# Kernel optimization log

Measured on AMD Instinct MI355X. Metric: run time of the kernel, lower is better.

## Reference

```python
import jax, jax.numpy as jnp
import numpy as np

K = 7            # neighbor volumes (NNN heads)
PS = 10          # patch size
ADJ = PS // 2    # patch anchor offset (use_adj)
WOFF = 29 // 2   # search window half-size (ws=29)
KSEARCH = 224    # hardcoded in forward
T, C, E, HH, WW = 1, 8, 8, 64, 64


def _box1(a, axis):
    # sliding-window sum of length PS anchored at i-ADJ, zero outside
    pw = [(0, 0)] * a.ndim
    pw[axis] = (ADJ, PS - 1 - ADJ)
    ap = jnp.pad(a, pw)
    c = jnp.cumsum(ap, axis=axis)
    zp = [(0, 0)] * a.ndim
    zp[axis] = (1, 0)
    c = jnp.pad(c, zp)
    n = a.shape[axis]
    return jax.lax.slice_in_dim(c, PS, PS + n, axis=axis) - jax.lax.slice_in_dim(c, 0, n, axis=axis)


def box_sum(a):
    return _box1(_box1(a, -2), -1)


def setup_inputs():
    key = jax.random.key(0)
    ks = jax.random.split(key, 5)
    x = jax.random.normal(ks[0], (T, C, HH, WW), jnp.float32)
    xe = jax.random.normal(ks[1], (T, E, HH, WW), jnp.float32)
    ye = jax.random.normal(ks[2], (T, E, HH, WW), jnp.float32)
    y = jax.random.normal(ks[3], (T, C, HH, WW), jnp.float32)
    log_temp = 0.1 * jax.random.normal(ks[4], (T, 1, HH, WW), jnp.float32)
    return {"x": x, "xe": xe, "ye": ye, "y": y, "log_temp": log_temp}


def reference(x, xe, ye, y, log_temp):
    pad = lambda a: jnp.pad(a, ((0, 0), (0, 0), (1, 1), (1, 1)))
    x, xe, ye, y, log_temp = pad(x), pad(xe), pad(ye), pad(y), pad(log_temp)
    H, W = x.shape[-2:]
    Q = H * W
    xe0, ye0 = xe[0], ye[0]
    # search window offsets (ws x ws)
    dy, dx = np.meshgrid(np.arange(-WOFF, WOFF + 1), np.arange(-WOFF, WOFF + 1), indexing='ij')
    dy = jnp.asarray(dy.ravel()); dx = jnp.asarray(dx.ravel())
    nW = dy.shape[0]  # 841
    # patch squared norms (zero padded patches)
    n2_q = box_sum((ye0 ** 2).sum(0))   # (H,W)
    n2_db = box_sum((xe0 ** 2).sum(0))  # (H,W)
    xep = jnp.pad(xe0, ((0, 0), (WOFF, WOFF), (WOFF, WOFF)))
    n2p = jnp.pad(n2_db, WOFF)
    def shifted(d):
        s = jax.lax.dynamic_slice(xep, (0, WOFF + d[0], WOFF + d[1]), (E, H, W))
        n = jax.lax.dynamic_slice(n2p, (WOFF + d[0], WOFF + d[1]), (H, W))
        return s, n
    xe_s, n2_s = jax.vmap(shifted)(jnp.stack([dy, dx], -1))  # (nW,E,H,W),(nW,H,W)
    cross = box_sum((ye0[None] * xe_s).sum(1))               # (nW,H,W)
    dist = n2_q[None] + n2_s - 2.0 * cross                   # L2^2, (nW,H,W)
    qy = jnp.arange(H)[:, None]; qx = jnp.arange(W)[None, :]
    valid = ((qy[None] + dy[:, None, None] >= 0) & (qy[None] + dy[:, None, None] < H)
             & (qx[None] + dx[:, None, None] >= 0) & (qx[None] + dx[:, None, None] < W))
    self_m = (dy == 0) & (dx == 0)  # remove_self
    dist = jnp.where(valid & ~self_m[:, None, None], dist, 1e10)
    dist = dist.transpose(1, 2, 0).reshape(Q, nW)
    negd, idx = jax.lax.top_k(-dist, KSEARCH)  # closest KSEARCH, negd = -L2
    # avg-pooled log temperature per query patch
    lt = (box_sum(log_temp[0, 0]) / (PS * PS)).reshape(Q)
    # NeuralNearestNeighbors: iterative continuous top-k relaxation
    logits = negd / jnp.exp(lt)[:, None]
    Ws = []
    for _ in range(K):
        w = jax.nn.softmax(logits, axis=-1)
        logits = logits + jnp.log(jnp.clip(1.0 - w, 1e-6, None))
        Ws.append(w)
    Wk = jnp.stack(Ws)  # (K,Q,KSEARCH)
    # absolute candidate coords
    qyf = jnp.repeat(jnp.arange(H), W); qxf = jnp.tile(jnp.arange(W), H)
    ny = qyf[:, None] + dy[idx]; nx = qxf[:, None] + dx[idx]  # (Q,KSEARCH)
    # weighted patch sum (gather per patch offset)
    xpad = jnp.pad(x[0], ((0, 0), (ADJ, PS - 1 - ADJ), (ADJ, PS - 1 - ADJ)))
    z = jnp.zeros((K, Q, C, PS, PS), x.dtype)
    for oy in range(PS):
        for ox in range(PS):
            vals = xpad[:, ny + oy, nx + ox]  # (C,Q,KSEARCH)
            z = z.at[:, :, :, oy, ox].set(jnp.einsum('kqj,cqj->kqc', Wk, vals))
    # fold with counting (iFoldz): overlap-add of patches + coverage counts
    zp = z.transpose(1, 0, 2, 3, 4).reshape(H, W, K * C, PS, PS)
    buf = jnp.zeros((K * C, H + PS - 1, W + PS - 1), x.dtype)
    cnt = jnp.zeros((H + PS - 1, W + PS - 1), x.dtype)
    for oy in range(PS):
        for ox in range(PS):
            buf = buf.at[:, oy:oy + H, ox:ox + W].add(zp[:, :, :, oy, ox].transpose(2, 0, 1))
            cnt = cnt.at[oy:oy + H, ox:ox + W].add(1.0)
    vid = buf[:, ADJ:ADJ + H, ADJ:ADJ + W]
    zvid = cnt[ADJ:ADJ + H, ADJ:ADJ + W]
    zagg = vid / zvid[None]
    zagg = zagg.reshape(T, K, C, H, W) - y.reshape(T, 1, C, H, W)
    zagg = zagg.reshape(T, K * C, H, W)
    out = jnp.concatenate([y, zagg], axis=1)[..., 1:-1, 1:-1]
    return out
```

## Files before the change

kernel.cpp:

```cpp
#include <hip/hip_runtime.h>
#include <hip/hip_bf16.h>

#define HP    66
#define QTOT  (HP*HP)
#define LSTR  67
#define NWIN  29
#define NW    (NWIN*NWIN)
#define KK    7
#define WOFF2 14
#define NZ    15
#define QB    8
#define QBN   545
#define NIT   27
#define NSEG3 198


__global__ __launch_bounds__(256) void k_prep1(const float* __restrict__ x,
    const float* __restrict__ xe, const float* __restrict__ ye,
    const float* __restrict__ lt, float* __restrict__ ws) {
  int p = blockIdx.x * 256 + threadIdx.x;
  if (p >= QTOT) return;
  int i = p / HP, j = p % HP;
  bool in = (i >= 1 && i < HP-1 && j >= 1 && j < HP-1);
  int src = (i-1)*64 + (j-1);
  float vy[8], vx[8], vv[8];
  float sy = 0.f, sx = 0.f;
#pragma unroll
  for (int e = 0; e < 8; ++e) {
    vy[e] = in ? ye[e*4096 + src] : 0.f;
    vx[e] = in ? xe[e*4096 + src] : 0.f;
    vv[e] = in ? x [e*4096 + src] : 0.f;
    sy += vy[e]*vy[e]; sx += vx[e]*vx[e];
  }
  float4* yp = (float4*)(ws + (size_t)p*8);
  float4* xp = (float4*)(ws + 8*QTOT + (size_t)p*8);
  float4* vp = (float4*)(ws + 16*QTOT + (size_t)p*8);
  yp[0] = make_float4(vy[0], vy[1], vy[2], vy[3]);
  yp[1] = make_float4(vy[4], vy[5], vy[6], vy[7]);
  xp[0] = make_float4(vx[0], vx[1], vx[2], vx[3]);
  xp[1] = make_float4(vx[4], vx[5], vx[6], vx[7]);
  vp[0] = make_float4(vv[0], vv[1], vv[2], vv[3]);
  vp[1] = make_float4(vv[4], vv[5], vv[6], vv[7]);
  ws[24*QTOT + p] = sy;
  ws[25*QTOT + p] = sx;
  ws[26*QTOT + p] = in ? lt[src] : 0.f;
}

__global__ __launch_bounds__(256) void k_prep2(float* __restrict__ ws) {
  int p = blockIdx.x * 256 + threadIdx.x;
  if (p >= QTOT) return;
  int i = p / HP, j = p % HP;
  const float* sqye = ws + 24*QTOT;
  const float* sqxe = ws + 25*QTOT;
  const float* lt66 = ws + 26*QTOT;
  float a = 0.f, b = 0.f, c = 0.f;
  for (int u = -5; u <= 4; ++u) {
    int ii = i + u; if (ii < 0 || ii >= HP) continue;
    for (int v = -5; v <= 4; ++v) {
      int jj = j + v; if (jj < 0 || jj >= HP) continue;
      int o = ii*HP + jj;
      a += sqye[o]; b += sqxe[o]; c += lt66[o];
    }
  }
  ws[27*QTOT + p] = a;
  ws[28*QTOT + p] = b;
  ws[29*QTOT + p] = c * 0.01f;
}

__global__ __launch_bounds__(256) void k_dist(const float* __restrict__ ws,
                                              float* __restrict__ dist) {
  __shared__ float s[HP*LSTR];
  __shared__ float h[HP*LSTR];
  int w = blockIdx.x, tid = threadIdx.x;
  int dy = w / NWIN - WOFF2, dx = w % NWIN - WOFF2;
  const float* yex = ws;
  const float* xex = ws + 8*QTOT;
  const float* n2q  = ws + 27*QTOT;
  const float* n2db = ws + 28*QTOT;
  for (int p = tid; p < QTOT; p += 256) {
    int i = p / HP, j = p % HP;
    int ii = i + dy, jj = j + dx;
    float sv = 0.f;
    if (ii >= 0 && ii < HP && jj >= 0 && jj < HP) {
      int p2 = ii*HP + jj;
      const float4* yp = (const float4*)(yex + (size_t)p*8);
      const float4* xp = (const float4*)(xex + (size_t)p2*8);
      float4 a0 = yp[0], a1 = yp[1], b0 = xp[0], b1 = xp[1];
      sv += a0.x*b0.x; sv += a0.y*b0.y; sv += a0.z*b0.z; sv += a0.w*b0.w;
      sv += a1.x*b1.x; sv += a1.y*b1.y; sv += a1.z*b1.z; sv += a1.w*b1.w;
    }
    s[i*LSTR + j] = sv;
  }
  __syncthreads();
  if (tid < NSEG3) {
    int row = tid % HP, seg = tid / HP, c0 = seg*22;
    const float* ar = s + row*LSTR;
    float* hr = h + row*LSTR;
    float w9[9]; float sum = 0.f;
#pragma unroll
    for (int t = 0; t < 9; ++t) {
      int jj = c0 - 5 + t;
      float v = (jj >= 0) ? ar[jj] : 0.f;
      w9[t] = v; sum += v;
    }
#pragma unroll
    for (int t = 0; t < 22; ++t) {
      int j = c0 + t, jn = j + 4;
      float nv = (jn < HP) ? ar[jn] : 0.f;
      sum += nv;
      hr[j] = sum;
      sum -= w9[t % 9];
      w9[t % 9] = nv;
    }
  }
  __syncthreads();
  if (tid < NSEG3) {
    int col = tid % HP, seg = tid / HP, r0 = seg*22;
    float w9[9]; float sum = 0.f;
#pragma unroll
    for (int t = 0; t < 9; ++t) {
      int ii = r0 - 5 + t;
      float v = (ii >= 0) ? h[ii*LSTR + col] : 0.f;
      w9[t] = v; sum += v;
    }
#pragma unroll
    for (int t = 0; t < 22; ++t) {
      int i = r0 + t, in2 = i + 4;
      float nv = (in2 < HP) ? h[in2*LSTR + col] : 0.f;
      sum += nv;
      float cr = sum;
      int p = i*HP + col;
      int ii = i + dy, jj = col + dx;
      bool valid = (ii >= 0 && ii < HP && jj >= 0 && jj < HP);
      float dv = 1e10f;
      if (valid && !(dy == 0 && dx == 0))
        dv = n2q[p] + n2db[ii*HP + jj] - 2.f * cr;
      dist[w*QTOT + p] = dv;
      sum -= w9[t % 9];
      w9[t % 9] = nv;
    }
  }
}

__global__ __launch_bounds__(256) void k_weights(const float* __restrict__ ws,
    const float* __restrict__ dist, __hip_bfloat16* __restrict__ wf) {
  __shared__ float mh[32], sh[32];
  int tid = threadIdx.x;
  int qq = tid & (QB-1);
  int qb = blockIdx.x;
  int q = qb * QB + qq;
  bool qok = q < QTOT;
  int qs = qok ? q : (QTOT - 1);
  int wg = tid >> 3;
  int wave = tid >> 6;
  float invT = __expf(-ws[29*QTOT + qs]);
  float lv[NIT];
#pragma unroll
  for (int it = 0; it < NIT; ++it) {
    int w = wg + it*32;
    lv[it] = (qok && w < NW) ? (-dist[w*QTOT + qs] * invT) : -3.0e38f;
  }
  for (int k = 0; k < KK; ++k) {
    float pm = -3.0e38f;
#pragma unroll
    for (int it = 0; it < NIT; ++it) pm = fmaxf(pm, lv[it]);
    pm = fmaxf(pm, __shfl_xor(pm, 8, 64));
    pm = fmaxf(pm, __shfl_xor(pm, 16, 64));
    pm = fmaxf(pm, __shfl_xor(pm, 32, 64));
    if ((tid & 63) < QB) mh[wave*QB + qq] = pm;
    __syncthreads();
    float m = fmaxf(fmaxf(mh[qq], mh[QB+qq]), fmaxf(mh[2*QB+qq], mh[3*QB+qq]));
    float psum = 0.f;
#pragma unroll
    for (int it = 0; it < NIT; ++it) psum += __expf(lv[it] - m);
    psum += __shfl_xor(psum, 8, 64);
    psum += __shfl_xor(psum, 16, 64);
    psum += __shfl_xor(psum, 32, 64);
    if ((tid & 63) < QB) sh[wave*QB + qq] = psum;
    __syncthreads();
    float invden = 1.0f / (sh[qq] + sh[QB+qq] + sh[2*QB+qq] + sh[3*QB+qq]);
    size_t bkq = ((size_t)k*QBN + qb)*NW;
#pragma unroll
    for (int it = 0; it < NIT; ++it) {
      int w = wg + it*32;
      if (qok && w < NW) {
        float wgt = __expf(lv[it] - m) * invden;
        wf[(bkq + w)*8 + qq] = __float2bfloat16(wgt);
        if (k < KK-1 && wgt > 1e-9f)
          lv[it] += __logf(fmaxf(1.f - wgt, 1e-6f));
      }
    }
    __syncthreads();
  }
}

__global__ __launch_bounds__(256) void k_boxw(__hip_bfloat16* __restrict__ wfp) {
  __shared__ uint4 au4[546];
  __shared__ float h[QTOT];
  int bid = blockIdx.x;
  int l = (bid & 7)*736 + (bid >> 3);
  if (l >= KK*NW) return;
  int k = l / NW, w = l % NW;
  uint4* u4 = (uint4*)wfp;
  size_t pb = ((size_t)k*QBN)*NW + w;
  int tid = threadIdx.x;
  for (int qb = tid; qb < QBN; qb += 256)
    au4[qb] = u4[pb + (size_t)qb*NW];
  if (tid < 8) ((unsigned short*)au4)[4356 + tid] = 0;
  __syncthreads();
  const unsigned short* a16 = (const unsigned short*)au4;
  if (tid < NSEG3) {
    int row = tid % HP, seg = tid / HP, c0 = seg*22;
    const unsigned short* ar = a16 + row*HP;
    float* hr = h + row*HP;
    float w9[9]; float sum = 0.f;
#pragma unroll
    for (int t = 0; t < 9; ++t) {
      int jj = c0 - 4 + t;
      float v = (jj >= 0) ? __uint_as_float((unsigned)ar[jj] << 16) : 0.f;
      w9[t] = v; sum += v;
    }
#pragma unroll
    for (int t = 0; t < 22; ++t) {
      int j = c0 + t, jn = j + 5;
      float nv = (jn < HP) ? __uint_as_float((unsigned)ar[jn] << 16) : 0.f;
      sum += nv;
      hr[j] = sum;
      sum -= w9[t % 9];
      w9[t % 9] = nv;
    }
  }
  __syncthreads();
  unsigned short* a16w = (unsigned short*)au4;
  if (tid < NSEG3) {
    int col = tid % HP, seg = tid / HP, r0 = seg*22;
    float w9[9]; float sum = 0.f;
#pragma unroll
    for (int t = 0; t < 9; ++t) {
      int ii = r0 - 4 + t;
      float v = (ii >= 0) ? h[ii*HP + col] : 0.f;
      w9[t] = v; sum += v;
    }
#pragma unroll
    for (int t = 0; t < 22; ++t) {
      int i = r0 + t, in2 = i + 5;
      float nv = (in2 < HP) ? h[in2*HP + col] : 0.f;
      sum += nv;
      a16w[i*HP + col] = __bfloat16_as_ushort(__float2bfloat16(sum));
      sum -= w9[t % 9];
      w9[t % 9] = nv;
    }
  }
  __syncthreads();
  for (int qb = tid; qb < QBN; qb += 256)
    u4[pb + (size_t)qb*NW] = au4[qb];
}

__global__ __launch_bounds__(256) void k_contract(const float* __restrict__ ws,
    const unsigned short* __restrict__ wfu, float* __restrict__ accb2) {
  __shared__ float xt[17][44][8];
  int t = blockIdx.x, z = blockIdx.y, k = blockIdx.z, tid = threadIdx.x;
  int I0 = (t >> 2) * 16, J0 = (t & 3) * 16;
  int dylo = -WOFF2 + 2*z;
  int gy0 = I0 + 1 + dylo, gx0 = J0 - 13;
  const float* x66i = ws + 16*QTOT;
  for (int idx = tid; idx < 17*44; idx += 256) {
    int r = idx / 44, cc = idx % 44;
    int gy = gy0 + r, gx = gx0 + cc;
    float4 v0 = make_float4(0.f,0.f,0.f,0.f), v1 = v0;
    if (gy >= 0 && gy < HP && gx >= 0 && gx < HP) {
      const float4* xp = (const float4*)(x66i + (size_t)(gy*HP + gx)*8);
      v0 = xp[0]; v1 = xp[1];
    }
    float4* d = (float4*)&xt[r][cc][0];
    d[0] = v0; d[1] = v1;
  }
  __syncthreads();
  int il = tid >> 4, jl = tid & 15;
  int I = I0 + 1 + il, J = J0 + 1 + jl;
  int pix = I*HP + J;
  int qb = pix >> 3, q7 = pix & 7;
  size_t cb = (((size_t)k*QBN + qb)*NW)*8 + q7;
  float acc[8];
#pragma unroll
  for (int c = 0; c < 8; ++c) acc[c] = 0.f;
  int ndd = (z == NZ-1) ? 1 : 2;
  for (int dd = 0; dd < ndd; ++dd) {
    int wrow = (dylo + dd + WOFF2) * NWIN;
    const unsigned short* wp = wfu + cb + (size_t)wrow*8;
    unsigned short wv[NWIN];
#pragma unroll
    for (int dxw = 0; dxw < NWIN; ++dxw) wv[dxw] = wp[dxw*8];
    int r = il + dd;
#pragma unroll
    for (int dxw = 0; dxw < NWIN; ++dxw) {
      float wgt = __uint_as_float((unsigned)wv[dxw] << 16);
      const float4* xr = (const float4*)&xt[r][jl + dxw][0];
      float4 x0 = xr[0], x1 = xr[1];
      acc[0] += wgt * x0.x; acc[1] += wgt * x0.y;
      acc[2] += wgt * x0.z; acc[3] += wgt * x0.w;
      acc[4] += wgt * x1.x; acc[5] += wgt * x1.y;
      acc[6] += wgt * x1.z; acc[7] += wgt * x1.w;
    }
  }
  int px64 = (I-1)*64 + (J-1);
#pragma unroll
  for (int c = 0; c < 8; ++c)
    accb2[((z*56 + k*8 + c)*4096) + px64] = acc[c];
}

__global__ __launch_bounds__(256) void k_final(const float* __restrict__ y,
    const float* __restrict__ accb2, float* __restrict__ out) {
  int idx = blockIdx.x * 256 + threadIdx.x;
  int ch = idx >> 12, px = idx & 4095;
  if (ch < 8) { out[idx] = y[ch*4096 + px]; return; }
  int kc = ch - 8, c = kc & 7;
  int i = px >> 6, j = px & 63;
  int I = i + 1, J = j + 1;
  int cy = min(I+5, HP-1) - max(I-4, 0) + 1;
  int cx = min(J+5, HP-1) - max(J-4, 0) + 1;
  float s = 0.f;
  for (int z = 0; z < NZ; ++z) s += accb2[(z*56 + kc)*4096 + px];
  out[idx] = s / (float)(cy*cx) - y[c*4096 + px];
}

extern "C" void kernel_launch(void* const* d_in, const int* in_sizes, int n_in,
                              void* d_out, int out_size, void* d_ws, size_t ws_size,
                              hipStream_t stream) {
  const float* x  = (const float*)d_in[0];
  const float* xe = (const float*)d_in[1];
  const float* ye = (const float*)d_in[2];
  const float* y  = (const float*)d_in[3];
  const float* lt = (const float*)d_in[4];
  float* ws   = (float*)d_ws;
  float* dist = ws + 30*QTOT;
  __hip_bfloat16* wf = (__hip_bfloat16*)(dist + (size_t)NW*QTOT);
  float* accb2 = dist;
  float* out = (float*)d_out;

  k_prep1<<<(QTOT + 255)/256, 256, 0, stream>>>(x, xe, ye, lt, ws);
  k_prep2<<<(QTOT + 255)/256, 256, 0, stream>>>(ws);
  k_dist<<<NW, 256, 0, stream>>>(ws, dist);
  k_weights<<<QBN, 256, 0, stream>>>(ws, dist, wf);
  k_boxw<<<KK*NW, 256, 0, stream>>>(wf);
  k_contract<<<dim3(16, NZ, KK), 256, 0, stream>>>(ws, (const unsigned short*)wf, accb2);
  k_final<<<out_size/256, 256, 0, stream>>>(y, accb2, out);
}
```

Measured before the change: 145.9 us.

## Batch four window offsets per k_boxw block with padded weight layout

The weight buffer's per-query-block stride is padded from 841 to 844 window offsets, with the padding zeroed in k_weights. Each k_boxw block now processes four adjacent offsets, so its global loads and stores cover 64 contiguous bytes instead of scattered 16-byte chunks, and the launch shrinks to about a quarter of the blocks. In exchange each block holds four planes in LDS (about 35 KB plus the float plane), which lowers occupancy, and it runs the four box filters one after another with extra barriers.

```diff
diff --git a/kernel.cpp b/kernel.cpp
--- a/kernel.cpp
+++ b/kernel.cpp
@@ -6,6 +6,8 @@
 #define LSTR  67
 #define NWIN  29
 #define NW    (NWIN*NWIN)
+#define NWP   844
+#define NG    211
 #define KK    7
 #define WOFF2 14
 #define NZ    15
@@ -153,6 +155,12 @@
   int qs = qok ? q : (QTOT - 1);
   int wg = tid >> 3;
   int wave = tid >> 6;
+  if (tid < 24) {
+    int wp2 = NW + (tid >> 3), q2 = tid & 7;
+#pragma unroll
+    for (int k = 0; k < KK; ++k)
+      wf[(((size_t)k*QBN + qb)*NWP + wp2)*8 + q2] = __float2bfloat16(0.f);
+  }
   float invT = __expf(-ws[29*QTOT + qs]);
   float lv[NIT];
 #pragma unroll
@@ -179,7 +187,7 @@
     if ((tid & 63) < QB) sh[wave*QB + qq] = psum;
     __syncthreads();
     float invden = 1.0f / (sh[qq] + sh[QB+qq] + sh[2*QB+qq] + sh[3*QB+qq]);
-    size_t bkq = ((size_t)k*QBN + qb)*NW;
+    size_t bkq = ((size_t)k*QBN + qb)*NWP;
 #pragma unroll
     for (int it = 0; it < NIT; ++it) {
       int w = wg + it*32;
@@ -195,65 +203,74 @@
 }
 
 __global__ __launch_bounds__(256) void k_boxw(__hip_bfloat16* __restrict__ wfp) {
-  __shared__ uint4 au4[546];
+  __shared__ uint4 au4[4][546];
   __shared__ float h[QTOT];
   int bid = blockIdx.x;
-  int l = (bid & 7)*736 + (bid >> 3);
-  if (l >= KK*NW) return;
-  int k = l / NW, w = l % NW;
+  int k = bid / NG, g = bid % NG;
+  int w0 = g * 4;
   uint4* u4 = (uint4*)wfp;
-  size_t pb = ((size_t)k*QBN)*NW + w;
+  size_t pb = ((size_t)k*QBN)*NWP + w0;
   int tid = threadIdx.x;
-  for (int qb = tid; qb < QBN; qb += 256)
-    au4[qb] = u4[pb + (size_t)qb*NW];
-  if (tid < 8) ((unsigned short*)au4)[4356 + tid] = 0;
+  for (int idx = tid; idx < QBN*4; idx += 256) {
+    int qb = idx >> 2, wl = idx & 3;
+    au4[wl][qb] = u4[pb + (size_t)qb*NWP + wl];
+  }
+  if (tid < 48) {
+    int pl = tid / 12, e = tid % 12;
+    ((unsigned short*)au4[pl])[4356 + e] = 0;
+  }
   __syncthreads();
-  const unsigned short* a16 = (const unsigned short*)au4;
-  if (tid < NSEG3) {
-    int row = tid % HP, seg = tid / HP, c0 = seg*22;
-    const unsigned short* ar = a16 + row*HP;
-    float* hr = h + row*HP;
-    float w9[9]; float sum = 0.f;
-#pragma unroll
-    for (int t = 0; t < 9; ++t) {
-      int jj = c0 - 4 + t;
-      float v = (jj >= 0) ? __uint_as_float((unsigned)ar[jj] << 16) : 0.f;
-      w9[t] = v; sum += v;
-    }
-#pragma unroll
-    for (int t = 0; t < 22; ++t) {
-      int j = c0 + t, jn = j + 5;
-      float nv = (jn < HP) ? __uint_as_float((unsigned)ar[jn] << 16) : 0.f;
-      sum += nv;
-      hr[j] = sum;
-      sum -= w9[t % 9];
-      w9[t % 9] = nv;
-    }
-  }
-  __syncthreads();
-  unsigned short* a16w = (unsigned short*)au4;
-  if (tid < NSEG3) {
-    int col = tid % HP, seg = tid / HP, r0 = seg*22;
-    float w9[9]; float sum = 0.f;
-#pragma unroll
-    for (int t = 0; t < 9; ++t) {
-      int ii = r0 - 4 + t;
-      float v = (ii >= 0) ? h[ii*HP + col] : 0.f;
-      w9[t] = v; sum += v;
-    }
-#pragma unroll
-    for (int t = 0; t < 22; ++t) {
-      int i = r0 + t, in2 = i + 5;
-      float nv = (in2 < HP) ? h[in2*HP + col] : 0.f;
-      sum += nv;
-      a16w[i*HP + col] = __bfloat16_as_ushort(__float2bfloat16(sum));
-      sum -= w9[t % 9];
-      w9[t % 9] = nv;
-    }
-  }
-  __syncthreads();
-  for (int qb = tid; qb < QBN; qb += 256)
-    u4[pb + (size_t)qb*NW] = au4[qb];
+#pragma unroll
+  for (int pl = 0; pl < 4; ++pl) {
+    const unsigned short* a16 = (const unsigned short*)au4[pl];
+    if (tid < NSEG3) {
+      int row = tid % HP, seg = tid / HP, c0 = seg*22;
+      const unsigned short* ar = a16 + row*HP;
+      float* hr = h + row*HP;
+      float w9[9]; float sum = 0.f;
+#pragma unroll
+      for (int t = 0; t < 9; ++t) {
+        int jj = c0 - 4 + t;
+        float v = (jj >= 0) ? __uint_as_float((unsigned)ar[jj] << 16) : 0.f;
+        w9[t] = v; sum += v;
+      }
+#pragma unroll
+      for (int t = 0; t < 22; ++t) {
+        int j = c0 + t, jn = j + 5;
+        float nv = (jn < HP) ? __uint_as_float((unsigned)ar[jn] << 16) : 0.f;
+        sum += nv;
+        hr[j] = sum;
+        sum -= w9[t % 9];
+        w9[t % 9] = nv;
+      }
+    }
+    __syncthreads();
+    unsigned short* a16w = (unsigned short*)au4[pl];
+    if (tid < NSEG3) {
+      int col = tid % HP, seg = tid / HP, r0 = seg*22;
+      float w9[9]; float sum = 0.f;
+#pragma unroll
+      for (int t = 0; t < 9; ++t) {
+        int ii = r0 - 4 + t;
+        float v = (ii >= 0) ? h[ii*HP + col] : 0.f;
+        w9[t] = v; sum += v;
+      }
+#pragma unroll
+      for (int t = 0; t < 22; ++t) {
+        int i = r0 + t, in2 = i + 5;
+        float nv = (in2 < HP) ? h[in2*HP + col] : 0.f;
+        sum += nv;
+        a16w[i*HP + col] = __bfloat16_as_ushort(__float2bfloat16(sum));
+        sum -= w9[t % 9];
+        w9[t % 9] = nv;
+      }
+    }
+    __syncthreads();
+  }
+  for (int idx = tid; idx < QBN*4; idx += 256) {
+    int qb = idx >> 2, wl = idx & 3;
+    u4[pb + (size_t)qb*NWP + wl] = au4[wl][qb];
+  }
 }
 
 __global__ __launch_bounds__(256) void k_contract(const float* __restrict__ ws,
@@ -280,7 +297,7 @@
   int I = I0 + 1 + il, J = J0 + 1 + jl;
   int pix = I*HP + J;
   int qb = pix >> 3, q7 = pix & 7;
-  size_t cb = (((size_t)k*QBN + qb)*NW)*8 + q7;
+  size_t cb = (((size_t)k*QBN + qb)*NWP)*8 + q7;
   float acc[8];
 #pragma unroll
   for (int c = 0; c < 8; ++c) acc[c] = 0.f;
@@ -342,7 +359,7 @@
   k_prep2<<<(QTOT + 255)/256, 256, 0, stream>>>(ws);
   k_dist<<<NW, 256, 0, stream>>>(ws, dist);
   k_weights<<<QBN, 256, 0, stream>>>(ws, dist, wf);
-  k_boxw<<<KK*NW, 256, 0, stream>>>(wf);
+  k_boxw<<<KK*NG, 256, 0, stream>>>(wf);
   k_contract<<<dim3(16, NZ, KK), 256, 0, stream>>>(ws, (const unsigned short*)wf, accb2);
   k_final<<<out_size/256, 256, 0, stream>>>(y, accb2, out);
 }
```

After: 166.2 us. +13.9%, slower.
